# Kernel optimization log

Measured on AMD Instinct MI355X. Metric: run time of the kernel, lower is better.

The kernel has to match this reference:

```python
import jax, jax.numpy as jnp
import numpy as np

MUL = 16          # env_embed_multiplicity
LAT = 128         # latent dim
NUM_LAYERS = 2
AVG_N = 20.0      # avg_num_neighbors -> env_sum_normalizations = rsqrt(avg_n)
P = 6.0           # PolynomialCutoff_p


def _mlp(x, w1, w2):
    # ScalarMLPFunction: Linear -> SiLU -> Linear
    return jax.nn.silu(x @ w1) @ w2


def _poly_cutoff(u, p=P):
    f = (1.0 - ((p + 1.0) * (p + 2.0) / 2.0) * u ** p
         + p * (p + 2.0) * u ** (p + 1.0)
         - (p * (p + 1.0) / 2.0) * u ** (p + 2.0))
    return jnp.where(u < 1.0, f, 0.0)


def _weighter(attr, w):
    # MakeWeightedChannels: attr [E,4] = 1x0e + 1x1o, w [E, MUL*2] (one weight per irrep per channel)
    w = w.reshape(-1, MUL, 2)
    fs = w[:, :, 0] * attr[:, 0:1]                    # [E,MUL] scalar channel
    fv = w[:, :, 1][:, :, None] * attr[:, None, 1:4]  # [E,MUL,3] vector channel
    return fs, fv


def _forward(edge_attr, node_attrs, edge_embed, edge_u,
             w2b1, w2b2, lat1_w1, lat1_w2, env0_w1, env0_w2, env1_w1, env1_w2,
             l2w0_w1, l2w0_w2, l2w1_w1, l2w1_w2, envlin_ws, envlin_wv,
             fl2w_w1, fl2w_w2, edge_index):
    E = edge_attr.shape[0]
    N = node_attrs.shape[0]
    center, neigh = edge_index[0], edge_index[1]
    cut = _poly_cutoff(edge_u)[:, None]               # per-layer cutoffs all = r_max
    norm = np.float32(1.0 / np.sqrt(AVG_N))
    inv_s3 = np.float32(1.0 / np.sqrt(3.0))           # CG norm for 1x1->0
    inv_s2 = np.float32(1.0 / np.sqrt(2.0))           # CG norm for 1x1->1 (cross)
    inv_sm = np.float32(1.0 / np.sqrt(MUL))

    # two-body latent: cat(center types, neighbor types, radial embedding)
    x2b = jnp.concatenate([node_attrs[center], node_attrs[neigh], edge_embed], axis=-1)
    lat = cut * _mlp(x2b, w2b1, w2b2)                 # [E,LAT]
    w0 = _mlp(lat, env0_w1, env0_w2)                  # [E,4*MUL] = edge-embed + env weights
    w_edge, w_env = w0[:, :2 * MUL], w0[:, 2 * MUL:]
    fs, fv = _weighter(edge_attr, w_edge)             # initial edge features (embed_initial_edge)

    latent_in = None
    for l in range(NUM_LAYERS):
        if l > 0:
            # latent resnet (update param = 0 -> sigmoid(0))
            new_lat = cut * _mlp(latent_in, lat1_w1, lat1_w2)
            a = np.float32(jax.nn.sigmoid(0.0))
            c_old = np.float32(1.0 / np.sqrt(a * a + 1.0))
            lat = c_old * lat + (a * c_old) * new_lat
            w_env = _mlp(lat, env1_w1, env1_w2)
        # weighted environment embedding: scatter-sum over neighbors, normalize
        es_e, ev_e = _weighter(edge_attr, w_env)
        env_s = jax.ops.segment_sum(es_e, center, num_segments=N) * norm   # [N,MUL]
        env_v = jax.ops.segment_sum(ev_e, center, num_segments=N) * norm   # [N,MUL,3]
        # env_linear (per-irrep channel mixing)
        env_s = (env_s @ envlin_ws[l]) * inv_sm
        env_v = jnp.einsum('nui,uv->nvi', env_v, envlin_wv[l]) * inv_sm
        es, ev = env_s[center], env_v[center]          # gather back to edges
        # channelwise ('uuu') tensor product, lmax=1: 2 scalar + 3 vector paths
        s1 = fs * es
        s2 = jnp.sum(fv * ev, axis=-1) * inv_s3
        v1 = fs[:, :, None] * ev
        v2 = fv * es[:, :, None]
        v3 = jnp.cross(fv, ev) * inv_s2
        scalars = jnp.stack([s1, s2], axis=-1).reshape(E, 2 * MUL)
        latent_in = jnp.concatenate([lat, scalars], axis=-1)      # [E, LAT+2*MUL]
        # per-edge generated linear (shared_weights=False)
        lw1, lw2 = (l2w0_w1, l2w0_w2) if l == 0 else (l2w1_w1, l2w1_w2)
        lw = _mlp(latent_in, lw1, lw2)                 # [E, 5*MUL*MUL]
        ws = lw[:, :2 * MUL * MUL].reshape(E, 2, MUL, MUL)
        wv = lw[:, 2 * MUL * MUL:].reshape(E, 3, MUL, MUL)
        S = jnp.stack([s1, s2], axis=1)                # [E,2,MUL]
        V = jnp.stack([v1, v2, v3], axis=1)            # [E,3,MUL,3]
        fs = jnp.einsum('epu,epuv->ev', S, ws) * np.float32(1.0 / np.sqrt(2.0 * MUL))
        fv = jnp.einsum('epui,epuv->evi', V, wv) * np.float32(1.0 / np.sqrt(3.0 * MUL))
    # final per-edge linear -> 1x1o output per edge
    fw = _mlp(latent_in, fl2w_w1, fl2w_w2)             # [E,MUL]
    return jnp.einsum('eu,eui->ei', fw, fv) * inv_sm   # [E,3]


def setup_inputs():
    key = jax.random.key(0)
    ks = jax.random.split(key, 24)
    E, N, T, B = 120000, 5000, 4, 8
    def w(k, i, o):
        return jax.random.normal(k, (i, o), jnp.float32) / np.float32(np.sqrt(i))
    return {
        'edge_attr': jax.random.normal(ks[0], (E, 4), jnp.float32),
        'node_attrs': jax.random.uniform(ks[1], (N, T), jnp.float32),
        'edge_embed': jax.random.uniform(ks[2], (E, B), jnp.float32),
        'edge_u': jax.random.uniform(ks[3], (E,), jnp.float32),
        'edge_index': jax.random.randint(ks[4], (2, E), 0, N, jnp.int32),
        'w2b1': w(ks[5], 2 * T + B, LAT), 'w2b2': w(ks[6], LAT, LAT),
        'lat1_w1': w(ks[7], LAT + 2 * MUL, LAT), 'lat1_w2': w(ks[8], LAT, LAT),
        'env0_w1': w(ks[9], LAT, LAT), 'env0_w2': w(ks[10], LAT, 4 * MUL),
        'env1_w1': w(ks[11], LAT, LAT), 'env1_w2': w(ks[12], LAT, 2 * MUL),
        'l2w0_w1': w(ks[13], LAT + 2 * MUL, LAT), 'l2w0_w2': w(ks[14], LAT, 5 * MUL * MUL),
        'l2w1_w1': w(ks[15], LAT + 2 * MUL, LAT), 'l2w1_w2': w(ks[16], LAT, 5 * MUL * MUL),
        'envlin_ws': jax.random.normal(ks[17], (NUM_LAYERS, MUL, MUL), jnp.float32),
        'envlin_wv': jax.random.normal(ks[18], (NUM_LAYERS, MUL, MUL), jnp.float32),
        'fl2w_w1': w(ks[19], LAT + 2 * MUL, LAT), 'fl2w_w2': w(ks[20], LAT, MUL),
    }


def reference(edge_attr, node_attrs, edge_embed, edge_u, edge_index,
              w2b1, w2b2, lat1_w1, lat1_w2, env0_w1, env0_w2, env1_w1, env1_w2,
              l2w0_w1, l2w0_w2, l2w1_w1, l2w1_w2, envlin_ws, envlin_wv,
              fl2w_w1, fl2w_w2):
    return _forward(edge_attr, node_attrs, edge_embed, edge_u,
                    w2b1, w2b2, lat1_w1, lat1_w2, env0_w1, env0_w2, env1_w1, env1_w2,
                    l2w0_w1, l2w0_w2, l2w1_w1, l2w1_w2, envlin_ws, envlin_wv,
                    fl2w_w1, fl2w_w2, edge_index)
```

## Files before the change

### kernel.cpp

```cpp
#include <hip/hip_runtime.h>

typedef _Float16 half_t;
typedef _Float16 half8 __attribute__((ext_vector_type(8)));
typedef _Float16 half2_t __attribute__((ext_vector_type(2)));
typedef float f32x16 __attribute__((ext_vector_type(16)));
typedef float f32x4 __attribute__((ext_vector_type(4)));

#define DEVINL __device__ __forceinline__

#define INV_S3 0.57735026918962576f
#define INV_S2 0.70710678118654752f
#define C_OLD  0.89442719099991588f
#define A_COLD 0.44721359549995794f
#define SC_ENV 0.05590169943749474f
#define SC_FS  0.17677669529663688f
#define SC_FV  0.14433756729740643f
#define SC_OUT 0.03608439182435161f
#define SSD 34
#define VPH 146

DEVINL float silu_f(float x) { return x / (1.f + __expf(-x)); }

DEVINL float poly_cut(float u) {
    float u2 = u * u, u4 = u2 * u2, u6 = u4 * u2;
    float f = 1.f - 28.f * u6 + 48.f * u6 * u - 21.f * u6 * u2;
    return (u < 1.f) ? f : 0.f;
}

DEVINL float pkh(float a, float b) {
    half2_t h; h[0] = (half_t)a; h[1] = (half_t)b;
    return __builtin_bit_cast(float, h);
}
DEVINL float2 uph(float p) {
    half2_t h = __builtin_bit_cast(half2_t, p);
    return make_float2((float)h[0], (float)h[1]);
}
DEVINL half8 mk8(const float* w) {
    f32x4 v = {w[0], w[1], w[2], w[3]};
    return __builtin_bit_cast(half8, v);
}
DEVINL float ld_pk2(const half_t* p) {
    half2_t h; h[0] = p[0]; h[1] = p[1];
    return __builtin_bit_cast(float, h);
}
DEVINL float ntl_f(const float* p) { return __builtin_nontemporal_load(p); }
DEVINL f32x4 ntl_f4(const void* p) {
    return __builtin_nontemporal_load((const f32x4*)p);
}
DEVINL f32x4 ld_f4(const void* p) { return *reinterpret_cast<const f32x4*>(p); }
DEVINL void st_h8(half8 v, half_t* p) { *reinterpret_cast<half8*>(p) = v; }
DEVINL void st_f4(const f32x4& v, float* p) { *reinterpret_cast<f32x4*>(p) = v; }

template <int KB>
DEVINL f32x16 colstage(const half_t* __restrict__ Wg, const float* B, int mtile,
                       int nl, int q) {
    const half_t* ap = Wg + (((size_t)mtile * KB + q) * 32 + nl) * 8;
    constexpr int H = KB / 2;
    f32x16 acc0;
#pragma unroll
    for (int i = 0; i < 16; ++i) acc0[i] = 0.f;
    if constexpr (H < 2) {
        half8 a = *reinterpret_cast<const half8*>(ap);
        acc0 = __builtin_amdgcn_mfma_f32_32x32x16_f16(a, mk8(B), acc0, 0, 0, 0);
        return acc0;
    } else {
        f32x16 acc1;
#pragma unroll
        for (int i = 0; i < 16; ++i) acc1[i] = 0.f;
#pragma unroll
        for (int h = 0; h + 1 < H; h += 2) {
            half8 a0 = *reinterpret_cast<const half8*>(ap + h * 512);
            half8 a1 = *reinterpret_cast<const half8*>(ap + (h + 1) * 512);
            acc0 = __builtin_amdgcn_mfma_f32_32x32x16_f16(a0, mk8(B + h * 4), acc0, 0, 0, 0);
            acc1 = __builtin_amdgcn_mfma_f32_32x32x16_f16(a1, mk8(B + (h + 1) * 4), acc1, 0, 0, 0);
        }
        if constexpr (H & 1) {
            half8 a = *reinterpret_cast<const half8*>(ap + (H - 1) * 512);
            acc0 = __builtin_amdgcn_mfma_f32_32x32x16_f16(a, mk8(B + (H - 1) * 4), acc0, 0, 0, 0);
        }
        return acc0 + acc1;
    }
}

template <int KB>
DEVINL f32x16 colstage_lds(const half_t* W, const float* B, int nl, int q) {
    const half_t* ap = W + (q * 32 + nl) * 8;
    constexpr int H = KB / 2;
    f32x16 acc0, acc1;
#pragma unroll
    for (int i = 0; i < 16; ++i) { acc0[i] = 0.f; acc1[i] = 0.f; }
#pragma unroll
    for (int h = 0; h + 1 < H; h += 2) {
        half8 a0 = *reinterpret_cast<const half8*>(ap + h * 512);
        half8 a1 = *reinterpret_cast<const half8*>(ap + (h + 1) * 512);
        acc0 = __builtin_amdgcn_mfma_f32_32x32x16_f16(a0, mk8(B + h * 4), acc0, 0, 0, 0);
        acc1 = __builtin_amdgcn_mfma_f32_32x32x16_f16(a1, mk8(B + (h + 1) * 4), acc1, 0, 0, 0);
    }
    if constexpr (H & 1) {
        half8 a = *reinterpret_cast<const half8*>(ap + (H - 1) * 512);
        acc0 = __builtin_amdgcn_mfma_f32_32x32x16_f16(a, mk8(B + (H - 1) * 4), acc0, 0, 0, 0);
    }
    return acc0 + acc1;
}

struct WFrag { half8 a[8]; };

DEVINL f32x16 mfma8w(const WFrag& f, const float* B) {
    f32x16 acc0, acc1;
#pragma unroll
    for (int i = 0; i < 16; ++i) { acc0[i] = 0.f; acc1[i] = 0.f; }
#pragma unroll
    for (int h = 0; h < 8; h += 2) {
        acc0 = __builtin_amdgcn_mfma_f32_32x32x16_f16(f.a[h], mk8(B + h * 4), acc0, 0, 0, 0);
        acc1 = __builtin_amdgcn_mfma_f32_32x32x16_f16(f.a[h + 1], mk8(B + (h + 1) * 4), acc1, 0, 0, 0);
    }
    return acc0 + acc1;
}

DEVINL void silu16(f32x16& a) {
#pragma unroll
    for (int i = 0; i < 16; ++i) a[i] = silu_f(a[i]);
}

DEVINL void d2b(const f32x16& d, int lane, int q, float* wA, float* wB) {
    float pk[8];
#pragma unroll
    for (int a2 = 0; a2 < 4; ++a2) {
        pk[a2 * 2 + 0] = pkh(d[4 * a2 + 0], d[4 * a2 + 1]);
        pk[a2 * 2 + 1] = pkh(d[4 * a2 + 2], d[4 * a2 + 3]);
    }
#pragma unroll
    for (int t = 0; t < 2; ++t) {
        float k0 = q ? pk[(2 * t + 1) * 2 + 0] : pk[(2 * t) * 2 + 0];
        float k1 = q ? pk[(2 * t + 1) * 2 + 1] : pk[(2 * t) * 2 + 1];
        float s0 = q ? pk[(2 * t) * 2 + 0] : pk[(2 * t + 1) * 2 + 0];
        float s1 = q ? pk[(2 * t) * 2 + 1] : pk[(2 * t + 1) * 2 + 1];
        float r0 = __shfl(s0, lane ^ 32, 64);
        float r1 = __shfl(s1, lane ^ 32, 64);
        float* w = t ? wB : wA;
        w[0] = q ? r0 : k0;
        w[1] = q ? r1 : k1;
        w[2] = q ? k0 : r0;
        w[3] = q ? k1 : r1;
    }
}

DEVINL void ld5(const f32x4* src, f32x4* st, int tid) {
#pragma unroll
    for (int k = 0; k < 5; ++k) st[k] = ld_f4(src + k * 128 + tid);
}
DEVINL void ld4(const f32x4* src, f32x4* st, int tid) {
#pragma unroll
    for (int k = 0; k < 4; ++k) st[k] = ld_f4(src + k * 128 + tid);
}
DEVINL void wr5(f32x4* dst, const f32x4* st, int tid) {
#pragma unroll
    for (int k = 0; k < 5; ++k) dst[k * 128 + tid] = st[k];
}
DEVINL void wr4(f32x4* dst, const f32x4* st, int tid) {
#pragma unroll
    for (int k = 0; k < 4; ++k) dst[k * 128 + tid] = st[k];
}

__global__ __launch_bounds__(256) void k_zero(float* __restrict__ p, int n) {
    int i = blockIdx.x * 256 + threadIdx.x;
    if (i < n) p[i] = 0.f;
}

struct PackArgs {
    const float* src[14];
    half_t* dst[14];
    int K[14];
    int N[14];
};

__global__ __launch_bounds__(256) void k_pack(PackArgs pa) {
    int mi = blockIdx.y;
    int K = pa.K[mi], N = pa.N[mi];
    int Npad = (N + 31) & ~31;
    int KB = K >> 3;
    int cells = KB * Npad;
    int cell = blockIdx.x * 256 + threadIdx.x;
    if (cell >= cells) return;
    int nn = cell & 31, r2 = cell >> 5;
    int kblk = r2 % KB, ntile = r2 / KB;
    int n = ntile * 32 + nn;
    const float* W = pa.src[mi];
    half8 v;
#pragma unroll
    for (int j = 0; j < 8; ++j) {
        int k = kblk * 8 + j;
        v[j] = (half_t)((n < N) ? W[k * N + n] : 0.f);
    }
    *reinterpret_cast<half8*>(pa.dst[mi] + (size_t)cell * 8) = v;
}

__global__ __launch_bounds__(256) void k_hist(const int* __restrict__ eidx,
                                              int* __restrict__ cnt, int E) {
    int e = blockIdx.x * 256 + threadIdx.x;
    if (e < E) atomicAdd(&cnt[eidx[e]], 1);
}

__global__ __launch_bounds__(1024) void k_scan(const int* __restrict__ cnt,
                                               int* __restrict__ start,
                                               int* __restrict__ cursor, int Nn) {
    __shared__ int sh[1024];
    const int t = threadIdx.x;
    const int C = 5;
    int base = t * C;
    int local[C];
    int s = 0;
#pragma unroll
    for (int j = 0; j < C; ++j) {
        int idx = base + j;
        int v = (idx < Nn) ? cnt[idx] : 0;
        local[j] = v;
        s += v;
    }
    sh[t] = s;
    __syncthreads();
    for (int off = 1; off < 1024; off <<= 1) {
        int v = (t >= off) ? sh[t - off] : 0;
        __syncthreads();
        sh[t] += v;
        __syncthreads();
    }
    int run = sh[t] - s;
#pragma unroll
    for (int j = 0; j < C; ++j) {
        int idx = base + j;
        if (idx < Nn) {
            start[idx] = run;
            cursor[idx] = run;
            run += local[j];
        }
    }
    if (t == 1023) start[Nn] = sh[1023];
}

__global__ __launch_bounds__(256) void k_bucket(const int* __restrict__ eidx,
                                                int* __restrict__ cursor,
                                                int* __restrict__ eord, int E) {
    int e = blockIdx.x * 256 + threadIdx.x;
    if (e < E) {
        int pos = atomicAdd(&cursor[eidx[e]], 1);
        eord[pos] = e;
    }
}

__global__ __launch_bounds__(128, 2) void k_edge_front(
    const float* __restrict__ g_ea, const float* __restrict__ g_na,
    const float* __restrict__ g_emb, const float* __restrict__ g_eu,
    const int* __restrict__ g_eidx,
    const half_t* __restrict__ b_w2b1, const half_t* __restrict__ b_w2b2,
    const half_t* __restrict__ b_e0w1, const half_t* __restrict__ b_e0w2,
    half_t* __restrict__ g_lat0, float* __restrict__ g_fs, float* __restrict__ g_fv,
    float* __restrict__ contrib, int E) {
    __shared__ f32x4 Wbuf[2][512];
    const int tid = threadIdx.x;
    const int lane = tid & 63, nl = lane & 31, q = lane >> 5;
    const int wid = tid >> 6;
    const int g = blockIdx.x * 2 + wid;
    const int e = g * 32 + nl;
    float4 ea = *reinterpret_cast<const float4*>(g_ea + e * 4);
    float cut = poly_cut(g_eu[e]);

    const f32x4* s_w2b2 = reinterpret_cast<const f32x4*>(b_w2b2);
    const f32x4* s_e0w1 = reinterpret_cast<const f32x4*>(b_e0w1);
    const f32x4* s_e0w2 = reinterpret_cast<const f32x4*>(b_e0w2);

    f32x4 st[4];
    ld4(s_w2b2, st, tid);

    float xw[4];
    if (q == 0) {
        int ce0 = g_eidx[e];
        int ne = g_eidx[E + e];
        float4 nc = *reinterpret_cast<const float4*>(g_na + ce0 * 4);
        float4 nn = *reinterpret_cast<const float4*>(g_na + ne * 4);
        xw[0] = pkh(nc.x, nc.y); xw[1] = pkh(nc.z, nc.w);
        xw[2] = pkh(nn.x, nn.y); xw[3] = pkh(nn.z, nn.w);
    } else {
        f32x4 m0 = ntl_f4(g_emb + e * 8);
        f32x4 m1 = ntl_f4(g_emb + e * 8 + 4);
        xw[0] = pkh(m0[0], m0[1]); xw[1] = pkh(m0[2], m0[3]);
        xw[2] = pkh(m1[0], m1[1]); xw[3] = pkh(m1[2], m1[3]);
    }

    float hB[32], lB[32];
#pragma unroll
    for (int c = 0; c < 4; ++c) {
        f32x16 d = colstage<2>(b_w2b1, xw, c, nl, q);
        silu16(d);
        d2b(d, lane, q, &hB[8 * c], &hB[8 * c + 4]);
    }

    wr4(&Wbuf[0][0], st, tid);
    __syncthreads();

    half_t* gl = g_lat0 + (size_t)g * 4096;
#pragma unroll
    for (int c = 0; c < 4; ++c) {
        if (c < 3) ld4(s_w2b2 + (size_t)(c + 1) * 512, st, tid);
        else       ld4(s_e0w1, st, tid);
        f32x16 d = colstage_lds<16>(
            reinterpret_cast<const half_t*>(&Wbuf[c & 1][0]), hB, nl, q);
#pragma unroll
        for (int i = 0; i < 16; ++i) d[i] *= cut;
        d2b(d, lane, q, &lB[8 * c], &lB[8 * c + 4]);
        st_h8(mk8(&lB[8 * c]), gl + ((4 * c + q) * 32 + nl) * 8);
        st_h8(mk8(&lB[8 * c + 4]), gl + ((4 * c + 2 + q) * 32 + nl) * 8);
        __builtin_amdgcn_sched_barrier(0);
        wr4(&Wbuf[(c + 1) & 1][0], st, tid);
        __syncthreads();
    }
#pragma unroll
    for (int c = 0; c < 4; ++c) {
        if (c < 3) ld4(s_e0w1 + (size_t)(c + 1) * 512, st, tid);
        else       ld4(s_e0w2, st, tid);
        f32x16 d = colstage_lds<16>(
            reinterpret_cast<const half_t*>(&Wbuf[c & 1][0]), lB, nl, q);
        silu16(d);
        d2b(d, lane, q, &hB[8 * c], &hB[8 * c + 4]);
        __builtin_amdgcn_sched_barrier(0);
        wr4(&Wbuf[(c + 1) & 1][0], st, tid);
        __syncthreads();
    }
    f32x16 d0, d1;
    {
        ld4(s_e0w2 + 512, st, tid);
        d0 = colstage_lds<16>(
            reinterpret_cast<const half_t*>(&Wbuf[0][0]), hB, nl, q);
        __builtin_amdgcn_sched_barrier(0);
        wr4(&Wbuf[1][0], st, tid);
        __syncthreads();
        d1 = colstage_lds<16>(
            reinterpret_cast<const half_t*>(&Wbuf[1][0]), hB, nl, q);
    }
    {
        float* cp = contrib + (size_t)e * 64;
#pragma unroll
        for (int r = 0; r < 16; ++r) {
            int f = (r & 3) + 8 * (r >> 2) + 4 * q;
            int u = f >> 1;
            float v0 = d0[r], v1 = d1[r];
            if ((f & 1) == 0) {
                g_fs[e * 16 + u] = v0 * ea.x;
                cp[u] = v1 * ea.x;
            } else {
                g_fv[e * 48 + u * 3 + 0] = v0 * ea.y;
                g_fv[e * 48 + u * 3 + 1] = v0 * ea.z;
                g_fv[e * 48 + u * 3 + 2] = v0 * ea.w;
                cp[16 + u * 3 + 0] = v1 * ea.y;
                cp[16 + u * 3 + 1] = v1 * ea.z;
                cp[16 + u * 3 + 2] = v1 * ea.w;
            }
        }
    }
}

__global__ __launch_bounds__(256) void k_node_agg(
    const int* __restrict__ start, const int* __restrict__ eord,
    const float* __restrict__ contrib, const float* __restrict__ wls,
    const float* __restrict__ wlv, float* __restrict__ ls,
    float* __restrict__ lv, int Nn) {
    __shared__ float rawsh[4][64];
    const int t = threadIdx.x & 63;
    const int sub = threadIdx.x >> 6;
    const int n = blockIdx.x * 4 + sub;
    float acc = 0.f;
    if (n < Nn) {
        int s = start[n], en = start[n + 1];
        for (int base = s; base < en; base += 64) {
            int m = en - base; if (m > 64) m = 64;
            int myord = (base + t < en) ? eord[base + t] : 0;
            for (int i = 0; i < m; ++i) {
                int e2 = __shfl(myord, i, 64);
                acc += contrib[(size_t)e2 * 64 + t];
            }
        }
    }
    rawsh[sub][t] = acc;
    __syncthreads();
    if (n < Nn) {
        const float* raws = rawsh[sub];
        if (t < 16) {
            float as = 0.f;
#pragma unroll
            for (int u = 0; u < 16; ++u) as = fmaf(raws[u], wls[u * 16 + t], as);
            ls[n * 16 + t] = as * SC_ENV;
        } else {
            int idx = t - 16;
            int v = idx / 3, c = idx - 3 * v;
            float a = 0.f;
#pragma unroll
            for (int u = 0; u < 16; ++u)
                a = fmaf(raws[16 + u * 3 + c], wlv[u * 16 + v], a);
            lv[n * 48 + v * 3 + c] = a * SC_ENV;
        }
    }
}

__global__ __launch_bounds__(128, 2) void k_foldlat(
    const float* __restrict__ g_ea, const float* __restrict__ g_eu,
    const int* __restrict__ g_eidx,
    const float* __restrict__ g_fs, const float* __restrict__ g_fv,
    float* __restrict__ gfs2, float* __restrict__ gfv2,
    const float* __restrict__ ls0, const float* __restrict__ lv0,
    const half_t* __restrict__ b_lat1w1, const half_t* __restrict__ b_lat1w2,
    const half_t* __restrict__ b_e1w1, const half_t* __restrict__ b_e1w2,
    const half_t* __restrict__ b_gw1, const half_t* __restrict__ b_gw2,
    const half_t* __restrict__ g_lat0, half_t* __restrict__ g_lat1,
    float* __restrict__ contrib, int nblk2, int E) {
    __shared__ __align__(16) char smem[39424];
    const int tid = threadIdx.x;
    const int lane = tid & 63, nl = lane & 31, q = lane >> 5;
    const int wid = tid >> 6;
    const int bid = blockIdx.x;

    if (bid < nblk2) {
        half_t* sS = reinterpret_cast<half_t*>(smem) + wid * (32 * SSD);
        half_t* Vsh = reinterpret_cast<half_t*>(smem + 4352) + wid * (32 * VPH);
        f32x4* Wb0 = reinterpret_cast<f32x4*>(smem + 23040);
        f32x4* Wb1 = Wb0 + 512;
        const int g = bid * 2 + wid;
        const int e = g * 32 + nl;
        int ce = g_eidx[e];

        const f32x4* gsrc = reinterpret_cast<const f32x4*>(b_gw2);
        f32x4 st[4];
#pragma unroll
        for (int k = 0; k < 4; ++k) st[k] = ld_f4(gsrc + k * 128 + tid);

#pragma unroll
        for (int mm = 0; mm < 8; ++mm) {
            int m = q * 8 + mm;
            float fs = ntl_f(g_fs + e * 16 + m);
            float fv0 = ntl_f(g_fv + e * 48 + m * 3 + 0);
            float fv1 = ntl_f(g_fv + e * 48 + m * 3 + 1);
            float fv2 = ntl_f(g_fv + e * 48 + m * 3 + 2);
            float es = ls0[ce * 16 + m];
            float ev0 = lv0[ce * 48 + m * 3 + 0];
            float ev1 = lv0[ce * 48 + m * 3 + 1];
            float ev2 = lv0[ce * 48 + m * 3 + 2];
            sS[nl * SSD + 2 * m + 0] = (half_t)(fs * es);
            sS[nl * SSD + 2 * m + 1] =
                (half_t)((fv0 * ev0 + fv1 * ev1 + fv2 * ev2) * INV_S3);
            half_t* vp = Vsh + nl * VPH;
            vp[m * 3 + 0] = (half_t)(fs * ev0);
            vp[m * 3 + 1] = (half_t)(fs * ev1);
            vp[m * 3 + 2] = (half_t)(fs * ev2);
            vp[(16 + m) * 3 + 0] = (half_t)(fv0 * es);
            vp[(16 + m) * 3 + 1] = (half_t)(fv1 * es);
            vp[(16 + m) * 3 + 2] = (half_t)(fv2 * es);
            vp[(32 + m) * 3 + 0] = (half_t)((fv1 * ev2 - fv2 * ev1) * INV_S2);
            vp[(32 + m) * 3 + 1] = (half_t)((fv2 * ev0 - fv0 * ev2) * INV_S2);
            vp[(32 + m) * 3 + 2] = (half_t)((fv0 * ev1 - fv1 * ev0) * INV_S2);
        }

        float lB[40];
        const half_t* gl0 = g_lat0 + (size_t)g * 4096;
#pragma unroll
        for (int h = 0; h < 8; ++h) {
            f32x4 v = ntl_f4(gl0 + ((2 * h + q) * 32 + nl) * 8);
            lB[h * 4 + 0] = v[0]; lB[h * 4 + 1] = v[1];
            lB[h * 4 + 2] = v[2]; lB[h * 4 + 3] = v[3];
        }
        __syncthreads();

#pragma unroll
        for (int j2 = 0; j2 < 4; ++j2) {
            lB[32 + j2] = ld_pk2(sS + nl * SSD + 8 * q + 2 * j2);
            lB[36 + j2] = ld_pk2(sS + nl * SSD + 16 + 8 * q + 2 * j2);
        }

        float hB[32];
#pragma unroll
        for (int c = 0; c < 4; ++c) {
            f32x16 d = colstage<20>(b_gw1, lB, c, nl, q);
            silu16(d);
            d2b(d, lane, q, &hB[8 * c], &hB[8 * c + 4]);
        }

#pragma unroll
        for (int k = 0; k < 4; ++k) Wb0[k * 128 + tid] = st[k];
        __syncthreads();

        float fsacc[8];
        float fvacc[8][3];
#pragma unroll
        for (int s = 0; s < 8; ++s) {
            fsacc[s] = 0.f;
            fvacc[s][0] = fvacc[s][1] = fvacc[s][2] = 0.f;
        }

        for (int c = 0; c < 40; ++c) {
            const int buf = c & 1;
            f32x4* cur = buf ? Wb1 : Wb0;
            f32x4* nxt = buf ? Wb0 : Wb1;
            if (c + 1 < 40) {
#pragma unroll
                for (int k = 0; k < 4; ++k)
                    st[k] = ld_f4(gsrc + (size_t)(c + 1) * 512 + k * 128 + tid);
            }
            f32x16 d;
            {
                WFrag f;
                const half_t* wp = reinterpret_cast<const half_t*>(cur);
#pragma unroll
                for (int h = 0; h < 8; ++h)
                    f.a[h] = *reinterpret_cast<const half8*>(
                        wp + ((q + 2 * h) * 32 + nl) * 8);
                d = mfma8w(f, hB);
            }
            if (c < 16) {
                int pu0 = 2 * c, pu1 = pu0 + 1;
                float S0 = (float)sS[nl * SSD + 2 * (pu0 & 15) + (pu0 >> 4)];
                float S1 = (float)sS[nl * SSD + 2 * (pu1 & 15) + (pu1 >> 4)];
#pragma unroll
                for (int r = 0; r < 16; ++r) {
                    int a = r >> 2, bb = r & 3, slot = (a & 1) * 4 + bb;
                    fsacc[slot] = fmaf((a < 2) ? S0 : S1, d[r], fsacc[slot]);
                }
            } else {
                int w0i = 2 * c - 32, w1i = w0i + 1;
                const half_t* vp = Vsh + nl * VPH;
                float V00 = (float)vp[w0i * 3], V01 = (float)vp[w0i * 3 + 1], V02 = (float)vp[w0i * 3 + 2];
                float V10 = (float)vp[w1i * 3], V11 = (float)vp[w1i * 3 + 1], V12 = (float)vp[w1i * 3 + 2];
#pragma unroll
                for (int r = 0; r < 16; ++r) {
                    int a = r >> 2, bb = r & 3, slot = (a & 1) * 4 + bb;
                    float x0 = (a < 2) ? V00 : V10;
                    float x1 = (a < 2) ? V01 : V11;
                    float x2 = (a < 2) ? V02 : V12;
                    fvacc[slot][0] = fmaf(x0, d[r], fvacc[slot][0]);
                    fvacc[slot][1] = fmaf(x1, d[r], fvacc[slot][1]);
                    fvacc[slot][2] = fmaf(x2, d[r], fvacc[slot][2]);
                }
            }
            __builtin_amdgcn_sched_barrier(0);
            if (c + 1 < 40) {
#pragma unroll
                for (int k = 0; k < 4; ++k) nxt[k * 128 + tid] = st[k];
            }
            __syncthreads();
        }

        {
            float* fp = gfs2 + e * 16 + 4 * q;
            f32x4 flo = {fsacc[0] * SC_FS, fsacc[1] * SC_FS,
                         fsacc[2] * SC_FS, fsacc[3] * SC_FS};
            f32x4 fhi = {fsacc[4] * SC_FS, fsacc[5] * SC_FS,
                         fsacc[6] * SC_FS, fsacc[7] * SC_FS};
            st_f4(flo, fp);
            st_f4(fhi, fp + 8);
            float t2[24];
#pragma unroll
            for (int s = 0; s < 4; ++s) {
#pragma unroll
                for (int c3 = 0; c3 < 3; ++c3) {
                    t2[s * 3 + c3] = fvacc[s][c3] * SC_FV;
                    t2[12 + s * 3 + c3] = fvacc[4 + s][c3] * SC_FV;
                }
            }
            float* vlo = gfv2 + e * 48 + 12 * q;
            float* vhi = gfv2 + e * 48 + 24 + 12 * q;
#pragma unroll
            for (int i = 0; i < 3; ++i) {
                f32x4 a = {t2[4 * i + 0], t2[4 * i + 1], t2[4 * i + 2], t2[4 * i + 3]};
                f32x4 b = {t2[12 + 4 * i + 0], t2[12 + 4 * i + 1],
                           t2[12 + 4 * i + 2], t2[12 + 4 * i + 3]};
                st_f4(a, vlo + 4 * i);
                st_f4(b, vhi + 4 * i);
            }
        }
    } else {
        half_t* sS = reinterpret_cast<half_t*>(smem) + wid * (32 * SSD);
        f32x4* Wb0 = reinterpret_cast<f32x4*>(smem + 4352);
        f32x4* Wb1 = Wb0 + 640;
        const int b = bid - nblk2;
        const int g = b * 2 + wid;
        const int e = g * 32 + nl;
        int ce = g_eidx[e];

        const f32x4* w11 = reinterpret_cast<const f32x4*>(b_lat1w1);
        const f32x4* w12 = reinterpret_cast<const f32x4*>(b_lat1w2);
        const f32x4* w21 = reinterpret_cast<const f32x4*>(b_e1w1);
        const f32x4* w22 = reinterpret_cast<const f32x4*>(b_e1w2);

        f32x4 st[5];
        ld5(w11, st, tid);

#pragma unroll
        for (int mm = 0; mm < 8; ++mm) {
            int m = q * 8 + mm;
            float fs = ntl_f(g_fs + e * 16 + m);
            float fv0 = ntl_f(g_fv + e * 48 + m * 3 + 0);
            float fv1 = ntl_f(g_fv + e * 48 + m * 3 + 1);
            float fv2 = ntl_f(g_fv + e * 48 + m * 3 + 2);
            float es = ls0[ce * 16 + m];
            float ev0 = lv0[ce * 48 + m * 3 + 0];
            float ev1 = lv0[ce * 48 + m * 3 + 1];
            float ev2 = lv0[ce * 48 + m * 3 + 2];
            sS[nl * SSD + 2 * m + 0] = (half_t)(fs * es);
            sS[nl * SSD + 2 * m + 1] =
                (half_t)((fv0 * ev0 + fv1 * ev1 + fv2 * ev2) * INV_S3);
        }

        float lB[40];
        const half_t* gl0 = g_lat0 + (size_t)g * 4096;
#pragma unroll
        for (int h = 0; h < 8; ++h) {
            f32x4 v = ntl_f4(gl0 + ((2 * h + q) * 32 + nl) * 8);
            lB[h * 4 + 0] = v[0]; lB[h * 4 + 1] = v[1];
            lB[h * 4 + 2] = v[2]; lB[h * 4 + 3] = v[3];
        }
        float4 ea = *reinterpret_cast<const float4*>(g_ea + e * 4);
        float cut = poly_cut(g_eu[e]);

        wr5(Wb0, st, tid);
        __syncthreads();

#pragma unroll
        for (int j2 = 0; j2 < 4; ++j2) {
            lB[32 + j2] = ld_pk2(sS + nl * SSD + 8 * q + 2 * j2);
            lB[36 + j2] = ld_pk2(sS + nl * SSD + 16 + 8 * q + 2 * j2);
        }

        float hB[32];
#pragma unroll
        for (int c = 0; c < 4; ++c) {
            if (c < 3) ld5(w11 + (size_t)(c + 1) * 640, st, tid);
            else       ld4(w12, st, tid);
            f32x16 d = colstage_lds<20>(
                reinterpret_cast<const half_t*>((c & 1) ? Wb1 : Wb0), lB, nl, q);
            silu16(d);
            d2b(d, lane, q, &hB[8 * c], &hB[8 * c + 4]);
            __builtin_amdgcn_sched_barrier(0);
            if (c < 3) wr5(((c + 1) & 1) ? Wb1 : Wb0, st, tid);
            else       wr4(((c + 1) & 1) ? Wb1 : Wb0, st, tid);
            __syncthreads();
        }
        half_t* gl1 = g_lat1 + (size_t)g * 4096;
        float sc = A_COLD * cut;
#pragma unroll
        for (int c = 0; c < 4; ++c) {
            if (c < 3) ld4(w12 + (size_t)(c + 1) * 512, st, tid);
            else       ld4(w21, st, tid);
            f32x16 d = colstage_lds<16>(
                reinterpret_cast<const half_t*>((c & 1) ? Wb1 : Wb0), hB, nl, q);
#pragma unroll
            for (int i = 0; i < 16; ++i) d[i] *= sc;
            float nw[8];
            d2b(d, lane, q, nw, nw + 4);
#pragma unroll
            for (int p = 0; p < 8; ++p) {
                float2 o = uph(lB[8 * c + p]);
                float2 nn2 = uph(nw[p]);
                lB[8 * c + p] = pkh(C_OLD * o.x + nn2.x, C_OLD * o.y + nn2.y);
            }
            st_h8(mk8(&lB[8 * c]), gl1 + ((4 * c + q) * 32 + nl) * 8);
            st_h8(mk8(&lB[8 * c + 4]), gl1 + ((4 * c + 2 + q) * 32 + nl) * 8);
            __builtin_amdgcn_sched_barrier(0);
            wr4(((c + 1) & 1) ? Wb1 : Wb0, st, tid);
            __syncthreads();
        }
#pragma unroll
        for (int c = 0; c < 4; ++c) {
            if (c == 3) ld4(w22, st, tid);
            f32x16 d = colstage_lds<16>(
                reinterpret_cast<const half_t*>((c & 1) ? Wb1 : Wb0), lB, nl, q);
            silu16(d);
            d2b(d, lane, q, &hB[8 * c], &hB[8 * c + 4]);
            if (c < 3) ld4(w21 + (size_t)(c + 1) * 512, st, tid);
            __builtin_amdgcn_sched_barrier(0);
            wr4(((c + 1) & 1) ? Wb1 : Wb0, st, tid);
            __syncthreads();
        }
        {
            f32x16 d = colstage_lds<16>(
                reinterpret_cast<const half_t*>(Wb0), hB, nl, q);
            float* cp = contrib + (size_t)e * 64;
#pragma unroll
            for (int r = 0; r < 16; ++r) {
                int f = (r & 3) + 8 * (r >> 2) + 4 * q;
                int u = f >> 1;
                float val = d[r];
                if ((f & 1) == 0) {
                    cp[u] = val * ea.x;
                } else {
                    cp[16 + u * 3 + 0] = val * ea.y;
                    cp[16 + u * 3 + 1] = val * ea.z;
                    cp[16 + u * 3 + 2] = val * ea.w;
                }
            }
        }
    }
}

__global__ __launch_bounds__(128, 2) void k_layer1(
    const int* __restrict__ g_eidx, const float* __restrict__ gfs2,
    const float* __restrict__ gfv2, const float* __restrict__ ls1,
    const float* __restrict__ lv1,
    const half_t* __restrict__ b_flw1, const half_t* __restrict__ b_flw2,
    const half_t* __restrict__ b_gw1, const half_t* __restrict__ b_gw2,
    const half_t* __restrict__ g_lat1, float* __restrict__ g_out, int E) {
    __shared__ half_t sS2[2][32 * SSD];
    __shared__ half_t Vsh2[2][32 * VPH];
    __shared__ f32x4 Wbuf[2][640];
    const int tid = threadIdx.x;
    const int lane = tid & 63, nl = lane & 31, q = lane >> 5;
    const int wid = tid >> 6;
    const int g = blockIdx.x * 2 + wid;
    const int e = g * 32 + nl;
    int ce = g_eidx[e];
    half_t* sS = sS2[wid];
    half_t* Vsh = Vsh2[wid];

    const f32x4* wf1 = reinterpret_cast<const f32x4*>(b_flw1);
    const f32x4* wf2 = reinterpret_cast<const f32x4*>(b_flw2);
    const f32x4* wg1 = reinterpret_cast<const f32x4*>(b_gw1);
    const f32x4* wg2 = reinterpret_cast<const f32x4*>(b_gw2);

    f32x4 st[5];
    ld5(wf1, st, tid);

#pragma unroll
    for (int mm = 0; mm < 8; ++mm) {
        int m = q * 8 + mm;
        float fs = ntl_f(gfs2 + e * 16 + m);
        float fv0 = ntl_f(gfv2 + e * 48 + m * 3 + 0);
        float fv1 = ntl_f(gfv2 + e * 48 + m * 3 + 1);
        float fv2 = ntl_f(gfv2 + e * 48 + m * 3 + 2);
        float es = ls1[ce * 16 + m];
        float ev0 = lv1[ce * 48 + m * 3 + 0];
        float ev1 = lv1[ce * 48 + m * 3 + 1];
        float ev2 = lv1[ce * 48 + m * 3 + 2];
        sS[nl * SSD + 2 * m + 0] = (half_t)(fs * es);
        sS[nl * SSD + 2 * m + 1] =
            (half_t)((fv0 * ev0 + fv1 * ev1 + fv2 * ev2) * INV_S3);
        half_t* vp = Vsh + nl * VPH;
        vp[m * 3 + 0] = (half_t)(fs * ev0);
        vp[m * 3 + 1] = (half_t)(fs * ev1);
        vp[m * 3 + 2] = (half_t)(fs * ev2);
        vp[(16 + m) * 3 + 0] = (half_t)(fv0 * es);
        vp[(16 + m) * 3 + 1] = (half_t)(fv1 * es);
        vp[(16 + m) * 3 + 2] = (half_t)(fv2 * es);
        vp[(32 + m) * 3 + 0] = (half_t)((fv1 * ev2 - fv2 * ev1) * INV_S2);
        vp[(32 + m) * 3 + 1] = (half_t)((fv2 * ev0 - fv0 * ev2) * INV_S2);
        vp[(32 + m) * 3 + 2] = (half_t)((fv0 * ev1 - fv1 * ev0) * INV_S2);
    }

    float lB[40];
    const half_t* gl1 = g_lat1 + (size_t)g * 4096;
#pragma unroll
    for (int h = 0; h < 8; ++h) {
        f32x4 v = ntl_f4(gl1 + ((2 * h + q) * 32 + nl) * 8);
        lB[h * 4 + 0] = v[0]; lB[h * 4 + 1] = v[1];
        lB[h * 4 + 2] = v[2]; lB[h * 4 + 3] = v[3];
    }

    wr5(&Wbuf[0][0], st, tid);
    __syncthreads();

#pragma unroll
    for (int j2 = 0; j2 < 4; ++j2) {
        lB[32 + j2] = ld_pk2(sS + nl * SSD + 8 * q + 2 * j2);
        lB[36 + j2] = ld_pk2(sS + nl * SSD + 16 + 8 * q + 2 * j2);
    }

    float hB[32];
#pragma unroll
    for (int c = 0; c < 4; ++c) {
        if (c < 3) ld5(wf1 + (size_t)(c + 1) * 640, st, tid);
        else       ld4(wf2, st, tid);
        f32x16 d = colstage_lds<20>(
            reinterpret_cast<const half_t*>(&Wbuf[c & 1][0]), lB, nl, q);
        silu16(d);
        d2b(d, lane, q, &hB[8 * c], &hB[8 * c + 4]);
        __builtin_amdgcn_sched_barrier(0);
        if (c < 3) wr5(&Wbuf[(c + 1) & 1][0], st, tid);
        else       wr4(&Wbuf[(c + 1) & 1][0], st, tid);
        __syncthreads();
    }
    float fw[8];
    {
        ld5(wg1, st, tid);
        f32x16 d = colstage_lds<16>(
            reinterpret_cast<const half_t*>(&Wbuf[0][0]), hB, nl, q);
#pragma unroll
        for (int r = 0; r < 8; ++r) fw[r] = d[r];
        __builtin_amdgcn_sched_barrier(0);
        wr5(&Wbuf[1][0], st, tid);
        __syncthreads();
    }
#pragma unroll
    for (int c = 0; c < 4; ++c) {
        if (c < 3) ld5(wg1 + (size_t)(c + 1) * 640, st, tid);
        else       ld4(wg2 + (size_t)16 * 512, st, tid);
        f32x16 d = colstage_lds<20>(
            reinterpret_cast<const half_t*>(&Wbuf[(c + 1) & 1][0]), lB, nl, q);
        silu16(d);
        d2b(d, lane, q, &hB[8 * c], &hB[8 * c + 4]);
        __builtin_amdgcn_sched_barrier(0);
        if (c < 3) wr5(&Wbuf[c & 1][0], st, tid);
        else       wr4(&Wbuf[c & 1][0], st, tid);
        __syncthreads();
    }
    float fvacc[8][3];
#pragma unroll
    for (int s = 0; s < 8; ++s) fvacc[s][0] = fvacc[s][1] = fvacc[s][2] = 0.f;
    for (int j = 0; j < 24; ++j) {
        const int pb = (j + 1) & 1;
        if (j < 23) {
#pragma unroll
            for (int k = 0; k < 4; ++k)
                st[k] = ld_f4(wg2 + (size_t)(17 + j) * 512 + k * 128 + tid);
        }
        f32x16 d;
        {
            WFrag f;
            const half_t* wp = reinterpret_cast<const half_t*>(&Wbuf[pb][0]);
#pragma unroll
            for (int h = 0; h < 8; ++h)
                f.a[h] = *reinterpret_cast<const half8*>(
                    wp + ((q + 2 * h) * 32 + nl) * 8);
            d = mfma8w(f, hB);
        }
        {
            int w0i = 2 * j, w1i = 2 * j + 1;
            const half_t* vp = Vsh + nl * VPH;
            float V00 = (float)vp[w0i * 3], V01 = (float)vp[w0i * 3 + 1], V02 = (float)vp[w0i * 3 + 2];
            float V10 = (float)vp[w1i * 3], V11 = (float)vp[w1i * 3 + 1], V12 = (float)vp[w1i * 3 + 2];
#pragma unroll
            for (int r = 0; r < 16; ++r) {
                int a = r >> 2, bb = r & 3, slot = (a & 1) * 4 + bb;
                float x0 = (a < 2) ? V00 : V10;
                float x1 = (a < 2) ? V01 : V11;
                float x2 = (a < 2) ? V02 : V12;
                fvacc[slot][0] = fmaf(x0, d[r], fvacc[slot][0]);
                fvacc[slot][1] = fmaf(x1, d[r], fvacc[slot][1]);
                fvacc[slot][2] = fmaf(x2, d[r], fvacc[slot][2]);
            }
        }
        __builtin_amdgcn_sched_barrier(0);
        if (j < 23) wr4(&Wbuf[pb ^ 1][0], st, tid);
        __syncthreads();
    }
    {
        float o0 = 0.f, o1 = 0.f, o2 = 0.f;
#pragma unroll
        for (int s = 0; s < 8; ++s) {
            o0 = fmaf(fw[s], fvacc[s][0], o0);
            o1 = fmaf(fw[s], fvacc[s][1], o1);
            o2 = fmaf(fw[s], fvacc[s][2], o2);
        }
        o0 += __shfl(o0, lane ^ 32, 64);
        o1 += __shfl(o1, lane ^ 32, 64);
        o2 += __shfl(o2, lane ^ 32, 64);
        if (q == 0) {
            g_out[e * 3 + 0] = o0 * SC_OUT;
            g_out[e * 3 + 1] = o1 * SC_OUT;
            g_out[e * 3 + 2] = o2 * SC_OUT;
        }
    }
}

extern "C" void kernel_launch(void* const* d_in, const int* in_sizes, int n_in,
                              void* d_out, int out_size, void* d_ws, size_t ws_size,
                              hipStream_t stream) {
    const float* g_ea = (const float*)d_in[0];
    const float* g_na = (const float*)d_in[1];
    const float* g_emb = (const float*)d_in[2];
    const float* g_eu = (const float*)d_in[3];
    const int* g_eidx = (const int*)d_in[4];
    const float* w2b1 = (const float*)d_in[5];
    const float* w2b2 = (const float*)d_in[6];
    const float* lat1w1 = (const float*)d_in[7];
    const float* lat1w2 = (const float*)d_in[8];
    const float* e0w1 = (const float*)d_in[9];
    const float* e0w2 = (const float*)d_in[10];
    const float* e1w1 = (const float*)d_in[11];
    const float* e1w2 = (const float*)d_in[12];
    const float* l2w0w1 = (const float*)d_in[13];
    const float* l2w0w2 = (const float*)d_in[14];
    const float* l2w1w1 = (const float*)d_in[15];
    const float* l2w1w2 = (const float*)d_in[16];
    const float* envws = (const float*)d_in[17];
    const float* envwv = (const float*)d_in[18];
    const float* flw1 = (const float*)d_in[19];
    const float* flw2 = (const float*)d_in[20];
    float* out = (float*)d_out;

    const int E = in_sizes[3];
    const int Nn = in_sizes[1] / 4;
    const int nblk = E / 32;
    const int nblk2 = nblk / 2;

    float* p = (float*)d_ws;
    float* gfs = p;  p += (size_t)E * 16;
    float* gfv = p;  p += (size_t)E * 48;
    float* gfs2 = p; p += (size_t)E * 16;
    float* gfv2 = p; p += (size_t)E * 48;
    float* contrib = p; p += (size_t)E * 64;
    float* ls0 = p;  p += (size_t)Nn * 16;
    float* lv0 = p;  p += (size_t)Nn * 48;
    float* ls1 = p;  p += (size_t)Nn * 16;
    float* lv1 = p;  p += (size_t)Nn * 48;
    half_t* hp = (half_t*)p;
    half_t* lat0h = hp; hp += (size_t)nblk * 4096;
    half_t* lat1h = hp; hp += (size_t)nblk * 4096;

    const int KN[14][2] = {{16, 128}, {128, 128}, {128, 128}, {128, 64},
                           {160, 128}, {128, 128}, {128, 128}, {128, 32},
                           {160, 128}, {128, 1280}, {160, 128}, {128, 1280},
                           {160, 128}, {128, 16}};
    const float* srcs[14] = {w2b1, w2b2, e0w1, e0w2, lat1w1, lat1w2, e1w1, e1w2,
                             l2w0w1, l2w0w2, l2w1w1, l2w1w2, flw1, flw2};
    PackArgs pa;
    half_t* bptr[14];
    for (int i = 0; i < 14; ++i) {
        int K = KN[i][0], N = KN[i][1];
        int Npad = (N + 31) & ~31;
        bptr[i] = hp;
        hp += (size_t)K * Npad;
        pa.src[i] = srcs[i];
        pa.dst[i] = bptr[i];
        pa.K[i] = K;
        pa.N[i] = N;
    }
    int* ip = (int*)hp;
    int* cnt = ip;    ip += Nn;
    int* cursor = ip; ip += Nn;
    int* startp = ip; ip += Nn + 1;
    int* eord = ip;   ip += E;

    k_pack<<<dim3(80, 14), 256, 0, stream>>>(pa);
    k_zero<<<(Nn + 255) / 256, 256, 0, stream>>>((float*)cnt, Nn);
    k_hist<<<(E + 255) / 256, 256, 0, stream>>>(g_eidx, cnt, E);
    k_scan<<<1, 1024, 0, stream>>>(cnt, startp, cursor, Nn);
    k_bucket<<<(E + 255) / 256, 256, 0, stream>>>(g_eidx, cursor, eord, E);

    k_edge_front<<<nblk2, 128, 0, stream>>>(g_ea, g_na, g_emb, g_eu, g_eidx,
                                            bptr[0], bptr[1], bptr[2], bptr[3],
                                            lat0h, gfs, gfv, contrib, E);
    const int nagg = (Nn + 3) / 4;
    k_node_agg<<<nagg, 256, 0, stream>>>(startp, eord, contrib, envws, envwv,
                                         ls0, lv0, Nn);
    k_foldlat<<<nblk, 128, 0, stream>>>(g_ea, g_eu, g_eidx, gfs, gfv, gfs2, gfv2,
                                        ls0, lv0, bptr[4], bptr[5], bptr[6],
                                        bptr[7], bptr[8], bptr[9], lat0h, lat1h,
                                        contrib, nblk2, E);
    k_node_agg<<<nagg, 256, 0, stream>>>(startp, eord, contrib, envws + 256,
                                         envwv + 256, ls1, lv1, Nn);
    k_layer1<<<nblk2, 128, 0, stream>>>(g_eidx, gfs2, gfv2, ls1, lv1,
                                        bptr[12], bptr[13], bptr[10], bptr[11],
                                        lat1h, out, E);
}
```

Baseline: 430.8 us.

## Widen k_foldlat blocks to four waves sharing staged weight tiles

k_foldlat now runs 256-thread blocks covering four 32-edge groups instead of two. Each weight tile staged in LDS is reused by twice as many waves, and each thread's share of the cooperative global-to-LDS copy is halved. Tail groups beyond the edge count are clamped to the last valid group, and their stores are masked. In exchange, LDS per block rises to about 62 KB, which may limit how many blocks fit per CU, and the partial last block does redundant work.

Measured after the change: 433.7 us. About the same (+0.7%).

```diff
diff --git a/kernel.cpp b/kernel.cpp
--- a/kernel.cpp
+++ b/kernel.cpp
@@ -160,6 +160,20 @@
 DEVINL void wr4(f32x4* dst, const f32x4* st, int tid) {
 #pragma unroll
     for (int k = 0; k < 4; ++k) dst[k * 128 + tid] = st[k];
+}
+DEVINL void ld512c(const f32x4* src, f32x4* st, int tid) {
+    st[0] = ld_f4(src + tid); st[1] = ld_f4(src + 256 + tid);
+}
+DEVINL void wr512c(f32x4* dst, const f32x4* st, int tid) {
+    dst[tid] = st[0]; dst[256 + tid] = st[1];
+}
+DEVINL void ld640c(const f32x4* src, f32x4* st, int tid) {
+    st[0] = ld_f4(src + tid); st[1] = ld_f4(src + 256 + tid);
+    if (tid < 128) st[2] = ld_f4(src + 512 + tid);
+}
+DEVINL void wr640c(f32x4* dst, const f32x4* st, int tid) {
+    dst[tid] = st[0]; dst[256 + tid] = st[1];
+    if (tid < 128) dst[512 + tid] = st[2];
 }
 
 __global__ __launch_bounds__(256) void k_zero(float* __restrict__ p, int n) {
@@ -401,7 +415,7 @@
     }
 }
 
-__global__ __launch_bounds__(128, 2) void k_foldlat(
+__global__ __launch_bounds__(256, 2) void k_foldlat(
     const float* __restrict__ g_ea, const float* __restrict__ g_eu,
     const int* __restrict__ g_eidx,
     const float* __restrict__ g_fs, const float* __restrict__ g_fv,
@@ -411,26 +425,27 @@
     const half_t* __restrict__ b_e1w1, const half_t* __restrict__ b_e1w2,
     const half_t* __restrict__ b_gw1, const half_t* __restrict__ b_gw2,
     const half_t* __restrict__ g_lat0, half_t* __restrict__ g_lat1,
-    float* __restrict__ contrib, int nblk2, int E) {
-    __shared__ __align__(16) char smem[39424];
+    float* __restrict__ contrib, int nb4, int ngrp, int E) {
+    __shared__ __align__(16) char smem[62464];
     const int tid = threadIdx.x;
     const int lane = tid & 63, nl = lane & 31, q = lane >> 5;
     const int wid = tid >> 6;
     const int bid = blockIdx.x;
 
-    if (bid < nblk2) {
+    if (bid < nb4) {
         half_t* sS = reinterpret_cast<half_t*>(smem) + wid * (32 * SSD);
-        half_t* Vsh = reinterpret_cast<half_t*>(smem + 4352) + wid * (32 * VPH);
-        f32x4* Wb0 = reinterpret_cast<f32x4*>(smem + 23040);
+        half_t* Vsh = reinterpret_cast<half_t*>(smem + 8704) + wid * (32 * VPH);
+        f32x4* Wb0 = reinterpret_cast<f32x4*>(smem + 46080);
         f32x4* Wb1 = Wb0 + 512;
-        const int g = bid * 2 + wid;
-        const int e = g * 32 + nl;
+        const int g = bid * 4 + wid;
+        const bool act = g < ngrp;
+        const int ga = act ? g : ngrp - 1;
+        const int e = ga * 32 + nl;
         int ce = g_eidx[e];
 
         const f32x4* gsrc = reinterpret_cast<const f32x4*>(b_gw2);
-        f32x4 st[4];
-#pragma unroll
-        for (int k = 0; k < 4; ++k) st[k] = ld_f4(gsrc + k * 128 + tid);
+        f32x4 st[2];
+        ld512c(gsrc, st, tid);
 
 #pragma unroll
         for (int mm = 0; mm < 8; ++mm) {
@@ -459,7 +474,7 @@
         }
 
         float lB[40];
-        const half_t* gl0 = g_lat0 + (size_t)g * 4096;
+        const half_t* gl0 = g_lat0 + (size_t)ga * 4096;
 #pragma unroll
         for (int h = 0; h < 8; ++h) {
             f32x4 v = ntl_f4(gl0 + ((2 * h + q) * 32 + nl) * 8);
@@ -482,8 +497,7 @@
             d2b(d, lane, q, &hB[8 * c], &hB[8 * c + 4]);
         }
 
-#pragma unroll
-        for (int k = 0; k < 4; ++k) Wb0[k * 128 + tid] = st[k];
+        wr512c(Wb0, st, tid);
         __syncthreads();
 
         float fsacc[8];
@@ -498,11 +512,7 @@
             const int buf = c & 1;
             f32x4* cur = buf ? Wb1 : Wb0;
             f32x4* nxt = buf ? Wb0 : Wb1;
-            if (c + 1 < 40) {
-#pragma unroll
-                for (int k = 0; k < 4; ++k)
-                    st[k] = ld_f4(gsrc + (size_t)(c + 1) * 512 + k * 128 + tid);
-            }
+            if (c + 1 < 40) ld512c(gsrc + (size_t)(c + 1) * 512, st, tid);
             f32x16 d;
             {
                 WFrag f;
@@ -539,14 +549,11 @@
                 }
             }
             __builtin_amdgcn_sched_barrier(0);
-            if (c + 1 < 40) {
-#pragma unroll
-                for (int k = 0; k < 4; ++k) nxt[k * 128 + tid] = st[k];
-            }
+            if (c + 1 < 40) wr512c(nxt, st, tid);
             __syncthreads();
         }
 
-        {
+        if (act) {
             float* fp = gfs2 + e * 16 + 4 * q;
             f32x4 flo = {fsacc[0] * SC_FS, fsacc[1] * SC_FS,
                          fsacc[2] * SC_FS, fsacc[3] * SC_FS};
@@ -576,11 +583,13 @@
         }
     } else {
         half_t* sS = reinterpret_cast<half_t*>(smem) + wid * (32 * SSD);
-        f32x4* Wb0 = reinterpret_cast<f32x4*>(smem + 4352);
+        f32x4* Wb0 = reinterpret_cast<f32x4*>(smem + 8704);
         f32x4* Wb1 = Wb0 + 640;
-        const int b = bid - nblk2;
-        const int g = b * 2 + wid;
-        const int e = g * 32 + nl;
+        const int b = bid - nb4;
+        const int g = b * 4 + wid;
+        const bool act = g < ngrp;
+        const int ga = act ? g : ngrp - 1;
+        const int e = ga * 32 + nl;
         int ce = g_eidx[e];
 
         const f32x4* w11 = reinterpret_cast<const f32x4*>(b_lat1w1);
@@ -588,8 +597,8 @@
         const f32x4* w21 = reinterpret_cast<const f32x4*>(b_e1w1);
         const f32x4* w22 = reinterpret_cast<const f32x4*>(b_e1w2);
 
-        f32x4 st[5];
-        ld5(w11, st, tid);
+        f32x4 st[3];
+        ld640c(w11, st, tid);
 
 #pragma unroll
         for (int mm = 0; mm < 8; ++mm) {
@@ -608,7 +617,7 @@
         }
 
         float lB[40];
-        const half_t* gl0 = g_lat0 + (size_t)g * 4096;
+        const half_t* gl0 = g_lat0 + (size_t)ga * 4096;
 #pragma unroll
         for (int h = 0; h < 8; ++h) {
             f32x4 v = ntl_f4(gl0 + ((2 * h + q) * 32 + nl) * 8);
@@ -618,7 +627,7 @@
         float4 ea = *reinterpret_cast<const float4*>(g_ea + e * 4);
         float cut = poly_cut(g_eu[e]);
 
-        wr5(Wb0, st, tid);
+        wr640c(Wb0, st, tid);
         __syncthreads();
 
 #pragma unroll
@@ -630,23 +639,23 @@
         float hB[32];
 #pragma unroll
         for (int c = 0; c < 4; ++c) {
-            if (c < 3) ld5(w11 + (size_t)(c + 1) * 640, st, tid);
-            else       ld4(w12, st, tid);
+            if (c < 3) ld640c(w11 + (size_t)(c + 1) * 640, st, tid);
+            else       ld512c(w12, st, tid);
             f32x16 d = colstage_lds<20>(
                 reinterpret_cast<const half_t*>((c & 1) ? Wb1 : Wb0), lB, nl, q);
             silu16(d);
             d2b(d, lane, q, &hB[8 * c], &hB[8 * c + 4]);
             __builtin_amdgcn_sched_barrier(0);
-            if (c < 3) wr5(((c + 1) & 1) ? Wb1 : Wb0, st, tid);
-            else       wr4(((c + 1) & 1) ? Wb1 : Wb0, st, tid);
+            if (c < 3) wr640c(((c + 1) & 1) ? Wb1 : Wb0, st, tid);
+            else       wr512c(((c + 1) & 1) ? Wb1 : Wb0, st, tid);
             __syncthreads();
         }
-        half_t* gl1 = g_lat1 + (size_t)g * 4096;
+        half_t* gl1 = g_lat1 + (size_t)ga * 4096;
         float sc = A_COLD * cut;
 #pragma unroll
         for (int c = 0; c < 4; ++c) {
-            if (c < 3) ld4(w12 + (size_t)(c + 1) * 512, st, tid);
-            else       ld4(w21, st, tid);
+            if (c < 3) ld512c(w12 + (size_t)(c + 1) * 512, st, tid);
+            else       ld512c(w21, st, tid);
             f32x16 d = colstage_lds<16>(
                 reinterpret_cast<const half_t*>((c & 1) ? Wb1 : Wb0), hB, nl, q);
 #pragma unroll
@@ -659,39 +668,43 @@
                 float2 nn2 = uph(nw[p]);
                 lB[8 * c + p] = pkh(C_OLD * o.x + nn2.x, C_OLD * o.y + nn2.y);
             }
-            st_h8(mk8(&lB[8 * c]), gl1 + ((4 * c + q) * 32 + nl) * 8);
-            st_h8(mk8(&lB[8 * c + 4]), gl1 + ((4 * c + 2 + q) * 32 + nl) * 8);
+            if (act) {
+                st_h8(mk8(&lB[8 * c]), gl1 + ((4 * c + q) * 32 + nl) * 8);
+                st_h8(mk8(&lB[8 * c + 4]), gl1 + ((4 * c + 2 + q) * 32 + nl) * 8);
+            }
             __builtin_amdgcn_sched_barrier(0);
-            wr4(((c + 1) & 1) ? Wb1 : Wb0, st, tid);
+            wr512c(((c + 1) & 1) ? Wb1 : Wb0, st, tid);
             __syncthreads();
         }
 #pragma unroll
         for (int c = 0; c < 4; ++c) {
-            if (c == 3) ld4(w22, st, tid);
+            if (c == 3) ld512c(w22, st, tid);
             f32x16 d = colstage_lds<16>(
                 reinterpret_cast<const half_t*>((c & 1) ? Wb1 : Wb0), lB, nl, q);
             silu16(d);
             d2b(d, lane, q, &hB[8 * c], &hB[8 * c + 4]);
-            if (c < 3) ld4(w21 + (size_t)(c + 1) * 512, st, tid);
+            if (c < 3) ld512c(w21 + (size_t)(c + 1) * 512, st, tid);
             __builtin_amdgcn_sched_barrier(0);
-            wr4(((c + 1) & 1) ? Wb1 : Wb0, st, tid);
+            wr512c(((c + 1) & 1) ? Wb1 : Wb0, st, tid);
             __syncthreads();
         }
         {
             f32x16 d = colstage_lds<16>(
                 reinterpret_cast<const half_t*>(Wb0), hB, nl, q);
-            float* cp = contrib + (size_t)e * 64;
-#pragma unroll
-            for (int r = 0; r < 16; ++r) {
-                int f = (r & 3) + 8 * (r >> 2) + 4 * q;
-                int u = f >> 1;
-                float val = d[r];
-                if ((f & 1) == 0) {
-                    cp[u] = val * ea.x;
-                } else {
-                    cp[16 + u * 3 + 0] = val * ea.y;
-                    cp[16 + u * 3 + 1] = val * ea.z;
-                    cp[16 + u * 3 + 2] = val * ea.w;
+            if (act) {
+                float* cp = contrib + (size_t)e * 64;
+#pragma unroll
+                for (int r = 0; r < 16; ++r) {
+                    int f = (r & 3) + 8 * (r >> 2) + 4 * q;
+                    int u = f >> 1;
+                    float val = d[r];
+                    if ((f & 1) == 0) {
+                        cp[u] = val * ea.x;
+                    } else {
+                        cp[16 + u * 3 + 0] = val * ea.y;
+                        cp[16 + u * 3 + 1] = val * ea.z;
+                        cp[16 + u * 3 + 2] = val * ea.w;
+                    }
                 }
             }
         }
@@ -896,6 +909,7 @@
     const int Nn = in_sizes[1] / 4;
     const int nblk = E / 32;
     const int nblk2 = nblk / 2;
+    const int nb4 = (nblk + 3) / 4;
 
     float* p = (float*)d_ws;
     float* gfs = p;  p += (size_t)E * 16;
@@ -947,10 +961,10 @@
     const int nagg = (Nn + 3) / 4;
     k_node_agg<<<nagg, 256, 0, stream>>>(startp, eord, contrib, envws, envwv,
                                          ls0, lv0, Nn);
-    k_foldlat<<<nblk, 128, 0, stream>>>(g_ea, g_eu, g_eidx, gfs, gfv, gfs2, gfv2,
-                                        ls0, lv0, bptr[4], bptr[5], bptr[6],
-                                        bptr[7], bptr[8], bptr[9], lat0h, lat1h,
-                                        contrib, nblk2, E);
+    k_foldlat<<<nb4 * 2, 256, 0, stream>>>(g_ea, g_eu, g_eidx, gfs, gfv, gfs2,
+                                           gfv2, ls0, lv0, bptr[4], bptr[5],
+                                           bptr[6], bptr[7], bptr[8], bptr[9],
+                                           lat0h, lat1h, contrib, nb4, nblk, E);
     k_node_agg<<<nagg, 256, 0, stream>>>(startp, eord, contrib, envws + 256,
                                          envwv + 256, ls1, lv1, Nn);
     k_layer1<<<nblk2, 128, 0, stream>>>(g_eidx, gfs2, gfv2, ls1, lv1,
```
